# Optimization experiments

Hardware: AMD Instinct MI355X
Metric: run time of the kernel (lower is better)

## Reference

```python
import jax, jax.numpy as jnp
from jax import lax
from jax.scipy.special import logsumexp
import numpy as np

N_NODES = 6144
N_EDGES = 98304
N_FEAT = 128
N_TPLT = 16
M_NODES = 10
N_CG = 5        # conditional-gradient (Frank-Wolfe) outer iterations
N_SINK = 50     # log-domain Sinkhorn iterations for the linearized OT subproblem


def setup_inputs() -> dict:
    key = jax.random.key(0)
    k1, k2, k3, k4 = jax.random.split(key, 4)
    x = jax.random.normal(k1, (N_NODES, N_FEAT), dtype=jnp.float32)
    edge_index = jax.random.randint(k2, (2, N_EDGES), 0, N_NODES, dtype=jnp.int64)
    # template_initialisation: uniform(0,1) adjacencies, symmetrized; normal features; zero q0/alpha0
    t_raw = jax.random.uniform(k3, (N_TPLT, M_NODES, M_NODES), dtype=jnp.float32)
    templates = 0.5 * (t_raw + jnp.transpose(t_raw, (0, 2, 1)))
    templates_features = jax.random.normal(k4, (N_TPLT, M_NODES, N_FEAT), dtype=jnp.float32)
    q0 = jnp.zeros((N_TPLT, M_NODES), dtype=jnp.float32)
    alpha0 = jnp.zeros((1,), dtype=jnp.float32)
    return {"x": x, "edge_index": edge_index, "templates": templates,
            "templates_features": templates_features, "q0": q0, "alpha0": alpha0}


def _sinkhorn_log(G, logp, logq, reg):
    """Log-domain Sinkhorn solving min <G,T> + reg*H(T) over U(p,q)."""
    K = -G / reg                         # [n, m]
    f0 = jnp.zeros_like(logp)

    def body(f, _):
        g = logq - logsumexp(K + f[:, None], axis=0)
        f = logp - logsumexp(K + g[None, :], axis=1)
        return f, None

    f, _ = lax.scan(body, f0, None, length=N_SINK)
    g = logq - logsumexp(K + f[:, None], axis=0)
    return jnp.exp(f[:, None] + K + g[None, :])


def _fgw2(M, C1, C2, p, q, alpha):
    """Fused Gromov-Wasserstein distance (square loss) via conditional gradient.
    M: [n,m] feature cost, C1: [n,n] graph structure, C2: [m,m] template structure."""
    # init_matrix (square loss): constC = f1(C1) p 1^T + 1 q^T f2(C2)^T
    constC = (C1 ** 2 @ p)[:, None] + (C2 ** 2 @ q)[None, :]   # [n, m]
    logp, logq = jnp.log(p), jnp.log(q)
    T0 = p[:, None] * q[None, :]

    def step(T, _):
        C1TC2 = C1 @ T @ C2                                   # [n, m] (dominant cost)
        grad = (1.0 - alpha) * M + alpha * 2.0 * (constC - 2.0 * C1TC2)
        reg = lax.stop_gradient(0.05 * jnp.max(jnp.abs(grad)) + 1e-8)
        Tn = _sinkhorn_log(grad, logp, logq, reg)             # linearized OT subproblem
        dT = Tn - T
        # exact line search for the quadratic objective along dT
        C1dTC2 = C1 @ dT @ C2
        a = -2.0 * alpha * jnp.sum(C1dTC2 * dT)
        b = (1.0 - alpha) * jnp.sum(M * dT) + alpha * (jnp.sum(constC * dT) - 4.0 * jnp.sum(C1TC2 * dT))
        tau = jnp.where(a > 0.0,
                        jnp.clip(-b / (2.0 * a + 1e-16), 0.0, 1.0),
                        jnp.where(a + b < 0.0, 1.0, 0.0))
        return T + tau * dT, None

    T, _ = lax.scan(step, T0, None, length=N_CG)
    gw = jnp.sum((constC - 2.0 * (C1 @ T @ C2)) * T)
    wass = jnp.sum(M * T)
    return (1.0 - alpha) * wass + alpha * gw


def reference(x, edge_index, templates, templates_features, q0, alpha0):
    alpha = jax.nn.sigmoid(alpha0)[0]
    q = jax.nn.softmax(q0, axis=1)                            # [T, m] template node weights
    n = x.shape[0]
    # dense adjacency from edge list (symmetrized)
    A = jnp.zeros((n, n), dtype=x.dtype).at[edge_index[0], edge_index[1]].set(1.0)
    C1 = jnp.maximum(A, A.T)                                  # [n, n]
    p = jnp.full((n,), 1.0 / n, dtype=x.dtype)
    # squared euclidean feature cost per template: [T, n, m]
    M = (jnp.sum(x ** 2, axis=1)[None, :, None]
         + jnp.sum(templates_features ** 2, axis=-1)[:, None, :]
         - 2.0 * jnp.einsum('nf,tmf->tnm', x, templates_features))
    dists = jax.vmap(_fgw2, in_axes=(0, None, 0, None, 0, None))(M, C1, templates, p, q, alpha)
    return dists                                              # [n_templates]
```

## Files before the change

### kernel.cpp

```cpp
#include <hip/hip_runtime.h>
#include <hip/hip_cooperative_groups.h>

namespace cgx = cooperative_groups;

static constexpr int NN  = 6144;
static constexpr int NE  = 98304;
static constexpr int NF  = 128;
static constexpr int NT  = 16;
static constexpr int MN  = 10;
static constexpr int NCG = 5;
static constexpr int NSK = 50;
static constexpr int WPR = NN / 32;
static constexpr int TPB = 768;
static constexpr int NBLK = 256;
static constexpr int RPT = NN / TPB;
static constexpr int NW  = TPB / 64;

static_assert(TPB * RPT == NN, "row mapping");

static constexpr size_t OFF_M   = 0;
static constexpr size_t OFF_T   = OFF_M  + (size_t)NT * NN * MN;
static constexpr size_t OFF_C   = OFF_T  + (size_t)NT * NN * 5;
static constexpr size_t OFF_D   = OFF_C  + (size_t)NT * NN * 5;
static constexpr size_t OFF_RS  = OFF_D  + (size_t)NT * NN * 5;
static constexpr size_t OFF_DEG = OFF_RS + NN;
static constexpr size_t OFF_CI  = OFF_DEG + NN;
static constexpr size_t OFF_NNZ = OFF_CI + NE;
static constexpr size_t OFF_HIST= OFF_NNZ + 1;
static constexpr size_t OFF_PERM= OFF_HIST + 256;

static constexpr int LDS_PL  = NN * 20;
static constexpr int LDS_SP  = TPB * 7 * 4;
static constexpr int LDS_DYN = LDS_PL + LDS_SP;

__device__ __forceinline__ unsigned f2bf(float f) {
    unsigned u = __float_as_uint(f);
    return (u + 0x7fffu + ((u >> 16) & 1u)) >> 16;
}
__device__ __forceinline__ unsigned packbf(float a, float b) { return f2bf(a) | (f2bf(b) << 16); }
__device__ __forceinline__ float bflo(unsigned w) { return __uint_as_float(w << 16); }
__device__ __forceinline__ float bfhi(unsigned w) { return __uint_as_float(w & 0xffff0000u); }

extern __shared__ char sMem[];

__global__ __launch_bounds__(TPB) void tfgw_kernel(
    const float* __restrict__ x, const void* __restrict__ eiv,
    const float* __restrict__ tpl, const float* __restrict__ tf,
    const float* __restrict__ q0, const float* __restrict__ a0,
    float* __restrict__ out, float* __restrict__ W)
{
    __shared__ float sC2[MN * MN];
    __shared__ float sq[MN], scq[MN], sqC2[MN], sNSQ[MN];
    __shared__ unsigned svp[5];
    __shared__ float sVf[MN];
    __shared__ float sCv[5];
    __shared__ float sRed[3 * NW];
    __shared__ float sBC[2];
    __shared__ float sDots[4];
    __shared__ int   sBin[256];

    const int tid = threadIdx.x;
    const int bid = blockIdx.x;

    unsigned* BM    = (unsigned*)(W + OFF_T);
    int* rowst      = (int*)(W + OFF_RS);
    int* degi       = (int*)(W + OFF_DEG);
    unsigned short* colix = (unsigned short*)(W + OFF_CI);
    int* nnzc       = (int*)(W + OFF_NNZ);
    int* histg      = (int*)(W + OFF_HIST);
    int* permg      = (int*)(W + OFF_PERM);
    float* Mw  = W + OFF_M;
    unsigned* Tg = (unsigned*)(W + OFF_T);
    unsigned* Cg = (unsigned*)(W + OFF_C);
    unsigned* Dg = (unsigned*)(W + OFF_D);

    uint4*    PL4x = (uint4*)sMem;
    unsigned* PL1x = (unsigned*)(sMem + NN * 16);
    unsigned* sPp  = (unsigned*)(sMem + LDS_PL);

    const float alpha  = 1.f / (1.f + __expf(-a0[0]));
    const float invn   = 1.f / (float)NN;
    const float alpha2 = 2.f * alpha;
    const float oma    = 1.f - alpha;

    cgx::grid_group grid = cgx::this_grid();

    for (int idx = bid * TPB + tid; idx < NN * WPR; idx += NBLK * TPB) BM[idx] = 0u;
    if (bid == 0) {
        if (tid < 256) histg[tid] = 0;
        if (tid == 0)  *nnzc = 0;
    }
    grid.sync();

    {
        const unsigned* uw = (const unsigned*)eiv;
        const bool is64 = (uw[1] == 0u && uw[3] == 0u && uw[5] == 0u);
        for (int e = bid * TPB + tid; e < NE; e += NBLK * TPB) {
            int s, d;
            if (is64) {
                s = (int)((const long long*)eiv)[e];
                d = (int)((const long long*)eiv)[NE + e];
            } else {
                s = ((const int*)eiv)[e];
                d = ((const int*)eiv)[NE + e];
            }
            atomicOr(&BM[(size_t)s * WPR + (d >> 5)], 1u << (d & 31));
            atomicOr(&BM[(size_t)d * WPR + (s >> 5)], 1u << (s & 31));
        }
        float* sTF = (float*)sMem;
        const int t = bid >> 4, rb = bid & 15;
        for (int k = tid; k < MN * NF; k += TPB) sTF[k] = tf[t * MN * NF + k];
        __syncthreads();
        if (tid < MN) {
            float s = 0.f;
            for (int k = 0; k < NF; ++k) { float v = sTF[tid * NF + k]; s += v * v; }
            sNSQ[tid] = s;
        }
        __syncthreads();
        if (tid < 384) {
            const int i = rb * 384 + tid;
            const float4* x4 = (const float4*)(x + (size_t)i * NF);
            const float4* t4 = (const float4*)sTF;
            float acc[MN]; float xn = 0.f;
            #pragma unroll
            for (int j = 0; j < MN; ++j) acc[j] = 0.f;
            for (int k4 = 0; k4 < NF / 4; ++k4) {
                float4 xv = x4[k4];
                xn += xv.x * xv.x + xv.y * xv.y + xv.z * xv.z + xv.w * xv.w;
                #pragma unroll
                for (int j = 0; j < MN; ++j) {
                    float4 tv = t4[j * (NF / 4) + k4];
                    acc[j] += xv.x * tv.x + xv.y * tv.y + xv.z * tv.z + xv.w * tv.w;
                }
            }
            float* Mrow = Mw + (size_t)t * NN * MN + (size_t)i * MN;
            #pragma unroll
            for (int j = 0; j < MN; ++j) Mrow[j] = xn + sNSQ[j] - 2.f * acc[j];
        }
    }
    grid.sync();

    {
        const int i = bid * TPB + tid;
        if (i < NN) {
            int cnt = 0;
            for (int w = 0; w < WPR; ++w) cnt += __popc(BM[(size_t)i * WPR + w]);
            int st = atomicAdd(nnzc, cnt);
            rowst[i] = st; degi[i] = cnt;
            atomicAdd(&histg[cnt > 255 ? 255 : cnt], 1);
            int p = st;
            for (int w = 0; w < WPR; ++w) {
                unsigned m = BM[(size_t)i * WPR + w];
                while (m) { int b = __ffs(m) - 1; m &= m - 1; colix[p++] = (unsigned short)((w << 5) + b); }
            }
        }
    }
    grid.sync();

    if (bid == 0) {
        if (tid == 0) {
            int run = 0;
            for (int b = 0; b < 256; ++b) { sBin[b] = run; run += histg[b]; }
        }
        __syncthreads();
        for (int i = tid; i < NN; i += TPB) {
            int d = degi[i]; if (d > 255) d = 255;
            permg[atomicAdd(&sBin[d], 1)] = i;
        }
    }
    grid.sync();

    if (bid >= NT) return;

    const int t = bid;
    float* Mb = Mw + (size_t)t * NN * MN;
    unsigned* Tb = Tg + (size_t)t * NN * 5;
    unsigned* Cb = Cg + (size_t)t * NN * 5;
    unsigned* Db = Dg + (size_t)t * NN * 5;

    if (tid == 0) {
        float qv[MN]; float qm = -1e30f;
        for (int j = 0; j < MN; ++j) { qv[j] = q0[t * MN + j]; qm = fmaxf(qm, qv[j]); }
        float qs = 0.f;
        for (int j = 0; j < MN; ++j) { qv[j] = __expf(qv[j] - qm); qs += qv[j]; }
        for (int j = 0; j < MN; ++j) { qv[j] /= qs; sq[j] = qv[j]; }
        for (int j = 0; j < MN; ++j) {
            float s2 = 0.f, s1 = 0.f;
            for (int k = 0; k < MN; ++k) {
                float cjk = tpl[t * MN * MN + j * MN + k];
                s2 += cjk * cjk * qv[k];
                s1 += tpl[t * MN * MN + k * MN + j] * qv[k];
            }
            scq[j] = s2; sqC2[j] = s1;
        }
    }
    for (int k = tid; k < MN * MN; k += TPB) sC2[k] = tpl[t * MN * MN + k];
    __syncthreads();

    float E[RPT][MN];
    float uu[RPT];
    float cp_[RPT];
    #pragma unroll
    for (int k = 0; k < RPT; ++k) cp_[k] = (float)degi[tid + k * TPB] * invn;

    for (int cgi = 0; cgi < NCG; ++cgi) {
        if (tid == 0) {
            float tau = 0.f;
            if (cgi > 0) {
                float a = -2.f * alpha * sDots[3];
                float b = oma * sDots[0] + alpha * (sDots[1] - 4.f * sDots[2]);
                if (a > 0.f) tau = fminf(fmaxf(-b / (2.f * a + 1e-16f), 0.f), 1.f);
                else         tau = (a + b < 0.f) ? 1.f : 0.f;
            }
            sBC[0] = tau;
        }
        __syncthreads();
        const float tau = sBC[0];
        if (cgi > 0 && tau == 0.f) break;

        float gmax = 0.f;
        #pragma unroll
        for (int k = 0; k < RPT; ++k) {
            const int r = tid + k * TPB;
            const float cp = cp_[k];
            const size_t b5 = (size_t)r * 5;
            float C[MN];
            if (cgi == 0) {
                #pragma unroll
                for (int h = 0; h < 5; ++h) {
                    unsigned tw = packbf(sq[2*h] * invn, sq[2*h+1] * invn);
                    unsigned cw = packbf(cp * sqC2[2*h], cp * sqC2[2*h+1]);
                    Tb[b5 + h] = tw; Cb[b5 + h] = cw;
                    C[2*h] = bflo(cw); C[2*h+1] = bfhi(cw);
                }
            } else {
                float dd[MN];
                uint4 a4 = PL4x[r]; unsigned b4 = PL1x[r];
                dd[0]=bflo(a4.x); dd[1]=bfhi(a4.x); dd[2]=bflo(a4.y); dd[3]=bfhi(a4.y);
                dd[4]=bflo(a4.z); dd[5]=bfhi(a4.z); dd[6]=bflo(a4.w); dd[7]=bfhi(a4.w);
                dd[8]=bflo(b4);   dd[9]=bfhi(b4);
                #pragma unroll
                for (int h = 0; h < 5; ++h) {
                    unsigned tw = Tb[b5 + h], cw = Cb[b5 + h], Dw = Db[b5 + h];
                    float T0 = bflo(tw) + tau * dd[2*h];
                    float T1 = bfhi(tw) + tau * dd[2*h+1];
                    float C0 = bflo(cw) + tau * bflo(Dw);
                    float C1v = bfhi(cw) + tau * bfhi(Dw);
                    unsigned ntw = packbf(T0, T1), ncw = packbf(C0, C1v);
                    Tb[b5 + h] = ntw; Cb[b5 + h] = ncw;
                    C[2*h] = bflo(ncw); C[2*h+1] = bfhi(ncw);
                }
            }
            #pragma unroll
            for (int h = 0; h < 5; ++h) {
                float2 mv = *(const float2*)(Mb + (size_t)r * MN + 2*h);
                float g0 = oma * mv.x + alpha2 * (cp + scq[2*h]   - 2.f * C[2*h]);
                float g1 = oma * mv.y + alpha2 * (cp + scq[2*h+1] - 2.f * C[2*h+1]);
                E[k][2*h] = g0; E[k][2*h+1] = g1;
                gmax = fmaxf(gmax, fmaxf(__builtin_fabsf(g0), __builtin_fabsf(g1)));
            }
        }
        #pragma unroll
        for (int d = 32; d; d >>= 1) gmax = fmaxf(gmax, __shfl_xor(gmax, d));
        if ((tid & 63) == 0) sRed[tid >> 6] = gmax;
        __syncthreads();
        if (tid == 0) {
            float m = sRed[0];
            for (int w = 1; w < NW; ++w) m = fmaxf(m, sRed[w]);
            sBC[1] = 1.f / (0.05f * m + 1e-8f);
        }
        __syncthreads();
        const float invreg = sBC[1];

        #pragma unroll
        for (int k = 0; k < RPT; ++k)
            #pragma unroll
            for (int j = 0; j < MN; ++j)
                E[k][j] = __expf(-E[k][j] * invreg);

        if (cgi == 0) {
            float a[MN];
            #pragma unroll
            for (int j = 0; j < MN; ++j) a[j] = 0.f;
            #pragma unroll
            for (int k = 0; k < RPT; ++k)
                #pragma unroll
                for (int j = 0; j < MN; ++j) a[j] += E[k][j];
            #pragma unroll
            for (int p = 0; p < 5; ++p) sPp[tid * 7 + p] = packbf(a[2*p], a[2*p+1]);
            __syncthreads();
            if (tid < 320) {
                const int p = tid >> 6, c = tid & 63;
                float s0 = 0.f, s1 = 0.f;
                #pragma unroll
                for (int kk = 0; kk < NW; ++kk) {
                    unsigned w = sPp[(c + (kk << 6)) * 7 + p];
                    s0 += bflo(w); s1 += bfhi(w);
                }
                #pragma unroll
                for (int d = 32; d; d >>= 1) { s0 += __shfl_xor(s0, d); s1 += __shfl_xor(s1, d); }
                if (c == 0) {
                    float v0 = sq[2*p] / s0, v1 = sq[2*p+1] / s1;
                    svp[p] = packbf(v0, v1);
                    sVf[2*p] = v0; sVf[2*p+1] = v1;
                }
            }
            __syncthreads();
        }

        for (int it = 1; it <= NSK; ++it) {
            float vv[MN];
            #pragma unroll
            for (int p = 0; p < 5; ++p) {
                unsigned w = svp[p];
                vv[2*p] = bflo(w); vv[2*p+1] = bfhi(w);
            }
            float a[MN];
            #pragma unroll
            for (int j = 0; j < MN; ++j) a[j] = 0.f;
            #pragma unroll
            for (int k = 0; k < RPT; ++k) {
                float R = 0.f;
                #pragma unroll
                for (int j = 0; j < MN; ++j) R += E[k][j] * vv[j];
                const float u = invn * __builtin_amdgcn_rcpf(R);
                uu[k] = u;
                #pragma unroll
                for (int j = 0; j < MN; ++j) a[j] += E[k][j] * u;
            }
            #pragma unroll
            for (int p = 0; p < 5; ++p) sPp[tid * 7 + p] = packbf(a[2*p], a[2*p+1]);
            __syncthreads();
            if (tid < 320) {
                const int p = tid >> 6, c = tid & 63;
                float s0 = 0.f, s1 = 0.f;
                #pragma unroll
                for (int kk = 0; kk < NW; ++kk) {
                    unsigned w = sPp[(c + (kk << 6)) * 7 + p];
                    s0 += bflo(w); s1 += bfhi(w);
                }
                #pragma unroll
                for (int d = 32; d; d >>= 1) { s0 += __shfl_xor(s0, d); s1 += __shfl_xor(s1, d); }
                if (c == 0) {
                    float v0 = sq[2*p] / s0, v1 = sq[2*p+1] / s1;
                    float o0 = sVf[2*p],    o1 = sVf[2*p+1];
                    sCv[p] = (__builtin_fabsf(v0 - o0) <= 2e-4f * v0 &&
                              __builtin_fabsf(v1 - o1) <= 2e-4f * v1) ? 1.f : 0.f;
                    sVf[2*p] = v0; sVf[2*p+1] = v1;
                    svp[p] = packbf(v0, v1);
                }
            }
            __syncthreads();
            if (sCv[0] + sCv[1] + sCv[2] + sCv[3] + sCv[4] == 5.f) break;
        }

        {
            float vv[MN];
            #pragma unroll
            for (int p = 0; p < 5; ++p) {
                unsigned w = svp[p];
                vv[2*p] = bflo(w); vv[2*p+1] = bfhi(w);
            }
            float sMdT = 0.f, sCdT = 0.f, sCTdT = 0.f;
            #pragma unroll
            for (int k = 0; k < RPT; ++k) {
                const int r = tid + k * TPB;
                const float cp = cp_[k];
                const size_t b5 = (size_t)r * 5;
                const float u = uu[k];
                float dd[MN];
                #pragma unroll
                for (int h = 0; h < 5; ++h) {
                    unsigned tw = Tb[b5 + h], cw = Cb[b5 + h];
                    float2 mv = *(const float2*)(Mb + (size_t)r * MN + 2*h);
                    float d0 = u * E[k][2*h]   * vv[2*h]   - bflo(tw);
                    float d1 = u * E[k][2*h+1] * vv[2*h+1] - bfhi(tw);
                    dd[2*h] = d0; dd[2*h+1] = d1;
                    sMdT  += mv.x * d0 + mv.y * d1;
                    sCdT  += (cp + scq[2*h]) * d0 + (cp + scq[2*h+1]) * d1;
                    sCTdT += bflo(cw) * d0 + bfhi(cw) * d1;
                }
                PL4x[r] = make_uint4(packbf(dd[0],dd[1]), packbf(dd[2],dd[3]),
                                     packbf(dd[4],dd[5]), packbf(dd[6],dd[7]));
                PL1x[r] = packbf(dd[8], dd[9]);
            }
            #pragma unroll
            for (int d = 32; d; d >>= 1) {
                sMdT  += __shfl_xor(sMdT, d);
                sCdT  += __shfl_xor(sCdT, d);
                sCTdT += __shfl_xor(sCTdT, d);
            }
            if ((tid & 63) == 0) {
                const int w = tid >> 6;
                sRed[w] = sMdT; sRed[NW + w] = sCdT; sRed[2*NW + w] = sCTdT;
            }
            __syncthreads();
            if (tid == 0) {
                float r0 = 0.f, r1 = 0.f, r2 = 0.f;
                for (int w = 0; w < NW; ++w) { r0 += sRed[w]; r1 += sRed[NW+w]; r2 += sRed[2*NW+w]; }
                sDots[0] = r0; sDots[1] = r1; sDots[2] = r2;
            }
            __syncthreads();
        }

        {
            float dot = 0.f;
            #pragma unroll
            for (int k = 0; k < RPT; ++k) {
                const int r = permg[tid + k * TPB];
                float y[MN];
                #pragma unroll
                for (int j = 0; j < MN; ++j) y[j] = 0.f;
                const int st = rowst[r], dg = degi[r];
                const unsigned short* cl = colix + st;
                int e = 0;
                for (; e + 2 <= dg; e += 2) {
                    const int j0 = cl[e], j1 = cl[e + 1];
                    uint4 qa = PL4x[j0]; unsigned ba = PL1x[j0];
                    uint4 qb = PL4x[j1]; unsigned bb = PL1x[j1];
                    y[0] += bflo(qa.x) + bflo(qb.x); y[1] += bfhi(qa.x) + bfhi(qb.x);
                    y[2] += bflo(qa.y) + bflo(qb.y); y[3] += bfhi(qa.y) + bfhi(qb.y);
                    y[4] += bflo(qa.z) + bflo(qb.z); y[5] += bfhi(qa.z) + bfhi(qb.z);
                    y[6] += bflo(qa.w) + bflo(qb.w); y[7] += bfhi(qa.w) + bfhi(qb.w);
                    y[8] += bflo(ba)   + bflo(bb);   y[9] += bfhi(ba)   + bfhi(bb);
                }
                if (e < dg) {
                    const int j0 = cl[e];
                    uint4 qa = PL4x[j0]; unsigned ba = PL1x[j0];
                    y[0] += bflo(qa.x); y[1] += bfhi(qa.x);
                    y[2] += bflo(qa.y); y[3] += bfhi(qa.y);
                    y[4] += bflo(qa.z); y[5] += bfhi(qa.z);
                    y[6] += bflo(qa.w); y[7] += bfhi(qa.w);
                    y[8] += bflo(ba);   y[9] += bfhi(ba);
                }
                uint4 q = PL4x[r]; unsigned b4 = PL1x[r];
                float dd[MN];
                dd[0]=bflo(q.x); dd[1]=bfhi(q.x); dd[2]=bflo(q.y); dd[3]=bfhi(q.y);
                dd[4]=bflo(q.z); dd[5]=bfhi(q.z); dd[6]=bflo(q.w); dd[7]=bfhi(q.w);
                dd[8]=bflo(b4);  dd[9]=bfhi(b4);
                #pragma unroll
                for (int h = 0; h < 5; ++h) {
                    float o0 = 0.f, o1 = 0.f;
                    #pragma unroll
                    for (int j = 0; j < MN; ++j) {
                        o0 += y[j] * sC2[j * MN + 2*h];
                        o1 += y[j] * sC2[j * MN + 2*h + 1];
                    }
                    dot += o0 * dd[2*h] + o1 * dd[2*h+1];
                    Db[(size_t)r * 5 + h] = packbf(o0, o1);
                }
            }
            #pragma unroll
            for (int d = 32; d; d >>= 1) dot += __shfl_xor(dot, d);
            if ((tid & 63) == 0) sRed[tid >> 6] = dot;
            __syncthreads();
            if (tid == 0) {
                float s = 0.f;
                for (int w = 0; w < NW; ++w) s += sRed[w];
                sDots[3] = s;
            }
            __syncthreads();
        }
    }

    if (tid == 0) {
        float a = -2.f * alpha * sDots[3];
        float b = oma * sDots[0] + alpha * (sDots[1] - 4.f * sDots[2]);
        float tau;
        if (a > 0.f) tau = fminf(fmaxf(-b / (2.f * a + 1e-16f), 0.f), 1.f);
        else         tau = (a + b < 0.f) ? 1.f : 0.f;
        sBC[0] = tau;
    }
    __syncthreads();
    {
        const float tau = sBC[0];
        float gw = 0.f, wass = 0.f;
        #pragma unroll
        for (int k = 0; k < RPT; ++k) {
            const int r = tid + k * TPB;
            const float cp = cp_[k];
            const size_t b5 = (size_t)r * 5;
            uint4 q = PL4x[r]; unsigned b4 = PL1x[r];
            float dd[MN];
            dd[0]=bflo(q.x); dd[1]=bfhi(q.x); dd[2]=bflo(q.y); dd[3]=bfhi(q.y);
            dd[4]=bflo(q.z); dd[5]=bfhi(q.z); dd[6]=bflo(q.w); dd[7]=bfhi(q.w);
            dd[8]=bflo(b4);  dd[9]=bfhi(b4);
            #pragma unroll
            for (int h = 0; h < 5; ++h) {
                unsigned tw = Tb[b5 + h], cw = Cb[b5 + h], Dw = Db[b5 + h];
                float2 mv = *(const float2*)(Mb + (size_t)r * MN + 2*h);
                float Tf0 = bflo(tw) + tau * dd[2*h];
                float Tf1 = bfhi(tw) + tau * dd[2*h+1];
                float Cf0 = bflo(cw) + tau * bflo(Dw);
                float Cf1 = bfhi(cw) + tau * bfhi(Dw);
                gw   += (cp + scq[2*h]   - 2.f * Cf0) * Tf0
                      + (cp + scq[2*h+1] - 2.f * Cf1) * Tf1;
                wass += mv.x * Tf0 + mv.y * Tf1;
            }
        }
        #pragma unroll
        for (int d = 32; d; d >>= 1) {
            gw   += __shfl_xor(gw, d);
            wass += __shfl_xor(wass, d);
        }
        if ((tid & 63) == 0) { sRed[tid >> 6] = gw; sRed[NW + (tid >> 6)] = wass; }
        __syncthreads();
        if (tid == 0) {
            float g = 0.f, ws = 0.f;
            for (int w = 0; w < NW; ++w) { g += sRed[w]; ws += sRed[NW + w]; }
            out[t] = oma * ws + alpha * g;
        }
    }
}

extern "C" void kernel_launch(void* const* d_in, const int* in_sizes, int n_in,
                              void* d_out, int out_size, void* d_ws, size_t ws_size,
                              hipStream_t stream) {
    const float* x   = (const float*)d_in[0];
    const void*  ei  = d_in[1];
    const float* tpl = (const float*)d_in[2];
    const float* tfp = (const float*)d_in[3];
    const float* q0  = (const float*)d_in[4];
    const float* a0  = (const float*)d_in[5];
    float* outp = (float*)d_out;
    float* Wp   = (float*)d_ws;
    (void)hipFuncSetAttribute(reinterpret_cast<const void*>(&tfgw_kernel),
                              hipFuncAttributeMaxDynamicSharedMemorySize, LDS_DYN);
    void* args[] = { &x, &ei, &tpl, &tfp, &q0, &a0, &outp, &Wp };
    hipLaunchCooperativeKernel(reinterpret_cast<const void*>(&tfgw_kernel),
                               dim3(NBLK), dim3(TPB), args, LDS_DYN, stream);
}
```

Baseline: 721.7 us.

## Pack Sinkhorn kernel matrix in bf16 registers and raise block size to 1024

The per-thread kernel matrix E is now stored as packed bf16 pairs instead of fp32, halving its register footprint. That saving is what lets the block grow from 768 to 1024 threads, so each thread handles fewer rows (6 instead of 8). Each Sinkhorn iteration now pays extra unpack instructions, and holding E in bf16 lowers precision, including the gradient before exponentiation. The larger block also adds more waves to each reduction step.

After: 965.0 us. +33.7%, slower.

```diff
diff --git a/kernel.cpp b/kernel.cpp
--- a/kernel.cpp
+++ b/kernel.cpp
@@ -11,7 +11,7 @@
 static constexpr int NCG = 5;
 static constexpr int NSK = 50;
 static constexpr int WPR = NN / 32;
-static constexpr int TPB = 768;
+static constexpr int TPB = 1024;
 static constexpr int NBLK = 256;
 static constexpr int RPT = NN / TPB;
 static constexpr int NW  = TPB / 64;
@@ -197,7 +197,7 @@
     for (int k = tid; k < MN * MN; k += TPB) sC2[k] = tpl[t * MN * MN + k];
     __syncthreads();
 
-    float E[RPT][MN];
+    unsigned Ep[RPT][5];
     float uu[RPT];
     float cp_[RPT];
     #pragma unroll
@@ -256,7 +256,7 @@
                 float2 mv = *(const float2*)(Mb + (size_t)r * MN + 2*h);
                 float g0 = oma * mv.x + alpha2 * (cp + scq[2*h]   - 2.f * C[2*h]);
                 float g1 = oma * mv.y + alpha2 * (cp + scq[2*h+1] - 2.f * C[2*h+1]);
-                E[k][2*h] = g0; E[k][2*h+1] = g1;
+                Ep[k][h] = packbf(g0, g1);
                 gmax = fmaxf(gmax, fmaxf(__builtin_fabsf(g0), __builtin_fabsf(g1)));
             }
         }
@@ -275,8 +275,10 @@
         #pragma unroll
         for (int k = 0; k < RPT; ++k)
             #pragma unroll
-            for (int j = 0; j < MN; ++j)
-                E[k][j] = __expf(-E[k][j] * invreg);
+            for (int h = 0; h < 5; ++h) {
+                unsigned w = Ep[k][h];
+                Ep[k][h] = packbf(__expf(-bflo(w) * invreg), __expf(-bfhi(w) * invreg));
+            }
 
         if (cgi == 0) {
             float a[MN];
@@ -285,7 +287,10 @@
             #pragma unroll
             for (int k = 0; k < RPT; ++k)
                 #pragma unroll
-                for (int j = 0; j < MN; ++j) a[j] += E[k][j];
+                for (int h = 0; h < 5; ++h) {
+                    unsigned w = Ep[k][h];
+                    a[2*h] += bflo(w); a[2*h+1] += bfhi(w);
+                }
             #pragma unroll
             for (int p = 0; p < 5; ++p) sPp[tid * 7 + p] = packbf(a[2*p], a[2*p+1]);
             __syncthreads();
@@ -320,13 +325,19 @@
             for (int j = 0; j < MN; ++j) a[j] = 0.f;
             #pragma unroll
             for (int k = 0; k < RPT; ++k) {
+                float e[MN];
+                #pragma unroll
+                for (int h = 0; h < 5; ++h) {
+                    unsigned w = Ep[k][h];
+                    e[2*h] = bflo(w); e[2*h+1] = bfhi(w);
+                }
                 float R = 0.f;
                 #pragma unroll
-                for (int j = 0; j < MN; ++j) R += E[k][j] * vv[j];
+                for (int j = 0; j < MN; ++j) R += e[j] * vv[j];
                 const float u = invn * __builtin_amdgcn_rcpf(R);
                 uu[k] = u;
                 #pragma unroll
-                for (int j = 0; j < MN; ++j) a[j] += E[k][j] * u;
+                for (int j = 0; j < MN; ++j) a[j] += e[j] * u;
             }
             #pragma unroll
             for (int p = 0; p < 5; ++p) sPp[tid * 7 + p] = packbf(a[2*p], a[2*p+1]);
@@ -372,9 +383,10 @@
                 #pragma unroll
                 for (int h = 0; h < 5; ++h) {
                     unsigned tw = Tb[b5 + h], cw = Cb[b5 + h];
+                    unsigned ew = Ep[k][h];
                     float2 mv = *(const float2*)(Mb + (size_t)r * MN + 2*h);
-                    float d0 = u * E[k][2*h]   * vv[2*h]   - bflo(tw);
-                    float d1 = u * E[k][2*h+1] * vv[2*h+1] - bfhi(tw);
+                    float d0 = u * bflo(ew) * vv[2*h]   - bflo(tw);
+                    float d1 = u * bfhi(ew) * vv[2*h+1] - bfhi(tw);
                     dd[2*h] = d0; dd[2*h+1] = d1;
                     sMdT  += mv.x * d0 + mv.y * d1;
                     sCdT  += (cp + scq[2*h]) * d0 + (cp + scq[2*h+1]) * d1;
```
